# Performance work log

Hardware: AMD Instinct MI355X
Metric: run time of the kernel (lower is better)

## Reference

```python
import jax, jax.numpy as jnp
import numpy as np

N = 20000      # nodes
E = 160000     # edges
IN = 128       # in_channels
H = 16         # heads
C = 32         # hidden_channels (per-head dim)
HC = H * C     # 512
ED = 93        # edge_dim
B = 64         # graphs in batch


def setup_inputs() -> dict:
    key = jax.random.key(0)
    ks = jax.random.split(key, 32)
    w = lambda i, shape: jax.random.normal(ks[i], shape, dtype=jnp.float32) * 0.05
    inp = {
        "x": jax.random.normal(ks[0], (N, IN), dtype=jnp.float32),
        "edge_attr": jax.random.normal(ks[1], (E, ED), dtype=jnp.float32),
        "edge_index": jax.random.randint(ks[2], (2, E), 0, N),
        # sorted batch assignment; every graph id 0..B-1 is present
        "batch": (jnp.arange(N) * B) // N,
        # transformer1: in=IN
        "t1_Wq": w(3, (IN, HC)), "t1_bq": jnp.zeros((HC,), jnp.float32),
        "t1_Wk": w(4, (IN, HC)), "t1_bk": jnp.zeros((HC,), jnp.float32),
        "t1_Wv": w(5, (IN, HC)), "t1_bv": jnp.zeros((HC,), jnp.float32),
        "t1_We": w(6, (ED, HC)),
        "t1_Ws": w(7, (IN, HC)), "t1_bs": jnp.zeros((HC,), jnp.float32),
        # transformer2: in=HC
        "t2_Wq": w(8, (HC, HC)), "t2_bq": jnp.zeros((HC,), jnp.float32),
        "t2_Wk": w(9, (HC, HC)), "t2_bk": jnp.zeros((HC,), jnp.float32),
        "t2_Wv": w(10, (HC, HC)), "t2_bv": jnp.zeros((HC,), jnp.float32),
        "t2_We": w(11, (ED, HC)),
        "t2_Ws": w(12, (HC, HC)), "t2_bs": jnp.zeros((HC,), jnp.float32),
        # MLP head: fc1 (hidden*32 -> hidden*8), fc2 (hidden*8 -> hidden)
        "fc1_W": w(13, (2 * HC, 8 * C)), "fc1_b": jnp.zeros((8 * C,), jnp.float32),
        "fc2_W": w(14, (8 * C, C)), "fc2_b": jnp.zeros((C,), jnp.float32),
    }
    return inp


def _tconv(x, src, dst, edge_attr, Wq, bq, Wk, bk, Wv, bv, We, Ws, bs):
    # PyG TransformerConv, concat=True, beta=False, root_weight=True
    n = x.shape[0]
    q = (x @ Wq + bq).reshape(n, H, C)
    k = (x @ Wk + bk).reshape(n, H, C)
    v = (x @ Wv + bv).reshape(n, H, C)
    e = (edge_attr @ We).reshape(-1, H, C)          # lin_edge has no bias
    kj = k[src] + e                                  # [E,H,C]
    alpha = jnp.einsum('ehc,ehc->eh', q[dst], kj) / jnp.sqrt(jnp.float32(C))
    # segment softmax over incoming edges of each destination node
    amax = jax.ops.segment_max(alpha, dst, num_segments=n)
    ex = jnp.exp(alpha - amax[dst])
    denom = jax.ops.segment_sum(ex, dst, num_segments=n)
    a = ex / denom[dst]                              # [E,H]
    msg = (v[src] + e) * a[:, :, None]               # [E,H,C]
    agg = jax.ops.segment_sum(msg.reshape(-1, HC), dst, num_segments=n)
    return agg + x @ Ws + bs                         # root/skip connection


def _pool(x, batch):
    counts = jax.ops.segment_sum(jnp.ones((x.shape[0],), x.dtype), batch, num_segments=B)
    mean = jax.ops.segment_sum(x, batch, num_segments=B) / jnp.maximum(counts, 1.0)[:, None]
    mx = jax.ops.segment_max(x, batch, num_segments=B)
    return jnp.concatenate([mean, mx], axis=1)


def reference(x, edge_attr, edge_index, batch,
              t1_Wq, t1_bq, t1_Wk, t1_bk, t1_Wv, t1_bv, t1_We, t1_Ws, t1_bs,
              t2_Wq, t2_bq, t2_Wk, t2_bk, t2_Wv, t2_bv, t2_We, t2_Ws, t2_bs,
              fc1_W, fc1_b, fc2_W, fc2_b):
    src, dst = edge_index[0], edge_index[1]
    x1 = jax.nn.leaky_relu(_tconv(x, src, dst, edge_attr,
                                  t1_Wq, t1_bq, t1_Wk, t1_bk, t1_Wv, t1_bv,
                                  t1_We, t1_Ws, t1_bs), negative_slope=0.2)
    x3 = _pool(x1, batch)
    x2 = jax.nn.leaky_relu(_tconv(x1, src, dst, edge_attr,
                                  t2_Wq, t2_bq, t2_Wk, t2_bk, t2_Wv, t2_bv,
                                  t2_We, t2_Ws, t2_bs), negative_slope=0.2)
    x4 = _pool(x2, batch)
    h = x3 + x4                                      # [B, 2*HC]
    h = jax.nn.relu(h @ fc1_W + fc1_b)               # dropout = identity (eval)
    out = h @ fc2_W + fc2_b                          # [B, C]
    return out
```

## Files before the change

### kernel.cpp

```cpp
#include <hip/hip_runtime.h>
#include <cstdint>
#include <cstddef>

#define N_NODES 20000
#define N_EDGES 160000
#define IN_CH   128
#define NH      16
#define CD      32
#define HC      512
#define ED      93
#define EDP     96
#define NB      64
#define NCAT    2048
#define NSLICE  8
#define DEGSLK  2048

typedef __attribute__((ext_vector_type(8))) short short8;
typedef __attribute__((ext_vector_type(4))) float f32x4;
typedef unsigned short ushort_t;


__device__ inline ushort_t f2bf(float f) {
    unsigned int u = __float_as_uint(f);
    u = (u + 0x7FFF + ((u >> 16) & 1)) >> 16;
    return (ushort_t)u;
}
__device__ inline float bf2f(ushort_t u) {
    return __uint_as_float((unsigned)u << 16);
}
__device__ inline void unpack8(uint4 u, float* o) {
    o[0] = bf2f((ushort_t)(u.x & 0xffff)); o[1] = bf2f((ushort_t)(u.x >> 16));
    o[2] = bf2f((ushort_t)(u.y & 0xffff)); o[3] = bf2f((ushort_t)(u.y >> 16));
    o[4] = bf2f((ushort_t)(u.z & 0xffff)); o[5] = bf2f((ushort_t)(u.z >> 16));
    o[6] = bf2f((ushort_t)(u.w & 0xffff)); o[7] = bf2f((ushort_t)(u.w >> 16));
}
__device__ inline uint4 packf8(const float* f) {
    uint4 u;
    u.x = (unsigned)f2bf(f[0]) | ((unsigned)f2bf(f[1]) << 16);
    u.y = (unsigned)f2bf(f[2]) | ((unsigned)f2bf(f[3]) << 16);
    u.z = (unsigned)f2bf(f[4]) | ((unsigned)f2bf(f[5]) << 16);
    u.w = (unsigned)f2bf(f[6]) | ((unsigned)f2bf(f[7]) << 16);
    return u;
}

__device__ inline void gload_lds16(const void* g, void* l) {
    __builtin_amdgcn_global_load_lds(
        (const __attribute__((address_space(1))) void*)g,
        (__attribute__((address_space(3))) void*)l, 16, 0, 0);
}

__global__ void k_zero_i(int* __restrict__ p, int n) {
    int i = blockIdx.x * blockDim.x + threadIdx.x;
    int stride = gridDim.x * blockDim.x;
    for (; i < n; i += stride) p[i] = 0;
}

__global__ void k_cvt_x(const float* __restrict__ in, ushort_t* __restrict__ out, int n8) {
    int i = blockIdx.x * blockDim.x + threadIdx.x;
    int stride = gridDim.x * blockDim.x;
    for (; i < n8; i += stride) {
        const float4* p = (const float4*)(in + (size_t)i * 8);
        float4 a = p[0], b = p[1];
        float f[8] = {a.x, a.y, a.z, a.w, b.x, b.y, b.z, b.w};
        *(uint4*)(out + (size_t)i * 8) = packf8(f);
    }
}

__global__ void k_cvt_ea(const float* __restrict__ in, const int* __restrict__ perm,
                         ushort_t* __restrict__ out) {
    int i = blockIdx.x * blockDim.x + threadIdx.x;
    int stride = gridDim.x * blockDim.x;
    int total = N_EDGES * EDP;
    for (; i < total; i += stride) {
        int p = i / EDP, k = i - p * EDP;
        int e = perm[p];
        out[i] = (k < ED) ? f2bf(in[(size_t)e * ED + k]) : (ushort_t)0;
    }
}

__global__ __launch_bounds__(256) void k_cvt_wtT(
    const float* __restrict__ W0, const float* __restrict__ W1,
    const float* __restrict__ W2, const float* __restrict__ W3,
    ushort_t* __restrict__ Wt, int K, int N, int Kp) {
    __shared__ float tile[32][33];
    int z = blockIdx.z;
    const float* W = (z == 0) ? W0 : (z == 1) ? W1 : (z == 2) ? W2 : W3;
    ushort_t* out = Wt + (size_t)z * N * Kp;
    int n0 = blockIdx.x << 5;
    int k0 = blockIdx.y << 5;
    int r = threadIdx.x >> 5;
    int c = threadIdx.x & 31;
#pragma unroll
    for (int rr = 0; rr < 4; ++rr) {
        int k = k0 + r + rr * 8;
        tile[r + rr * 8][c] = (k < K) ? W[(size_t)k * N + n0 + c] : 0.f;
    }
    __syncthreads();
#pragma unroll
    for (int rr = 0; rr < 4; ++rr) {
        int n = n0 + r + rr * 8;
        out[(size_t)n * Kp + k0 + c] = f2bf(tile[c][r + rr * 8]);
    }
}

__global__ void k_bcat2(
    const float* __restrict__ b0q, const float* __restrict__ b0k,
    const float* __restrict__ b0v, const float* __restrict__ b0s,
    const float* __restrict__ b1q, const float* __restrict__ b1k,
    const float* __restrict__ b1v, const float* __restrict__ b1s,
    float* __restrict__ out) {
    int i = blockIdx.x * blockDim.x + threadIdx.x;
    if (i >= 2 * NCAT) return;
    int l = i >> 11, j = i & (NCAT - 1);
    int s = j >> 9, jj = j & 511;
    const float* b = (l == 0)
        ? ((s == 0) ? b0q : (s == 1) ? b0k : (s == 2) ? b0v : b0s)
        : ((s == 0) ? b1q : (s == 1) ? b1k : (s == 2) ? b1v : b1s);
    out[i] = b[jj];
}


__global__ void k_hist(const int* __restrict__ dst, int* __restrict__ deg) {
    int i = blockIdx.x * blockDim.x + threadIdx.x;
    if (i < N_EDGES) atomicAdd(&deg[dst[i]], 1);
}

__global__ __launch_bounds__(1024) void k_scan(const int* __restrict__ deg,
                                               int* __restrict__ rowptr,
                                               int* __restrict__ cursor) {
    __shared__ int part[1024];
    int t = threadIdx.x;
    int base = t * 20;
    int loc[20];
    int s = 0;
#pragma unroll
    for (int i = 0; i < 20; ++i) {
        int idx = base + i;
        int v = (idx < N_NODES) ? deg[idx] : 0;
        loc[i] = s; s += v;
    }
    part[t] = s;
    __syncthreads();
    for (int off = 1; off < 1024; off <<= 1) {
        int v = (t >= off) ? part[t - off] : 0;
        __syncthreads();
        part[t] += v;
        __syncthreads();
    }
    int pre = (t > 0) ? part[t - 1] : 0;
#pragma unroll
    for (int i = 0; i < 20; ++i) {
        int idx = base + i;
        if (idx < N_NODES) {
            int v = pre + loc[i];
            rowptr[idx] = v;
            cursor[idx] = v;
        }
    }
    if (t == 1023) rowptr[N_NODES] = part[1023];
}

__global__ void k_scatter(const int* __restrict__ src, const int* __restrict__ dst,
                          int* __restrict__ cursor, int* __restrict__ perm,
                          int* __restrict__ psrc) {
    int i = blockIdx.x * blockDim.x + threadIdx.x;
    if (i >= N_EDGES) return;
    int d = dst[i];
    int p = atomicAdd(&cursor[d], 1);
    perm[p] = i;
    psrc[p] = src[i];
}


__global__ __launch_bounds__(256) void k_mega(
    const ushort_t* __restrict__ A, const ushort_t* __restrict__ Bt,
    const float* __restrict__ bias, ushort_t* __restrict__ Yb,
    int M, int K, int N, int nq,
    const ushort_t* __restrict__ Ab, const ushort_t* __restrict__ Bte,
    ushort_t* __restrict__ Ybe, int ec, int neg) {
    __shared__ char smem[49152];
    int tid  = threadIdx.x;
    int lane = tid & 63, wave = tid >> 6;
    int l15 = lane & 15, lg = lane >> 4;
    int wm = (wave >> 1) * 64, wn = (wave & 1) * 64;

    if (blockIdx.x < nq) {
        char* As = smem;
        char* Bs = smem + 16384;
        int nt = N >> 7;
        int bid = blockIdx.x;
        int wg;
        if ((nq & 7) == 0) { int cpx = nq >> 3; wg = (bid & 7) * cpx + (bid >> 3); }
        else wg = bid;
        int bm = (wg / nt) * 128, bn = (wg % nt) * 128;

        f32x4 acc[4][4] = {};

        int sr = lane >> 3;
        int su = lane & 7;
        int gu = su ^ sr;

        for (int k0 = 0; k0 < K; k0 += 64) {
#pragma unroll
            for (int i = 0; i < 4; ++i) {
                int rloc = wave * 32 + i * 8;
                int row = rloc + sr;
                if (bm + row < M)
                    gload_lds16(A + (size_t)(bm + row) * K + k0 + gu * 8, As + rloc * 128);
                gload_lds16(Bt + (size_t)(bn + row) * K + k0 + gu * 8, Bs + rloc * 128);
            }
            __syncthreads();

#pragma unroll
            for (int ks = 0; ks < 2; ++ks) {
                short8 af[4], bfr[4];
#pragma unroll
                for (int mr = 0; mr < 4; ++mr) {
                    int r = wm + mr * 16 + l15;
                    af[mr] = *(const short8*)(As + r * 128 + (((ks * 4 + lg) ^ (r & 7)) << 4));
                }
#pragma unroll
                for (int nc = 0; nc < 4; ++nc) {
                    int r = wn + nc * 16 + l15;
                    bfr[nc] = *(const short8*)(Bs + r * 128 + (((ks * 4 + lg) ^ (r & 7)) << 4));
                }
#pragma unroll
                for (int mr = 0; mr < 4; ++mr)
#pragma unroll
                    for (int nc = 0; nc < 4; ++nc)
                        acc[mr][nc] = __builtin_amdgcn_mfma_f32_16x16x32_bf16(
                            af[mr], bfr[nc], acc[mr][nc], 0, 0, 0);
            }
            __syncthreads();
        }

        char* Cs = smem;
#pragma unroll
        for (int mr = 0; mr < 4; ++mr) {
#pragma unroll
            for (int nc = 0; nc < 4; ++nc) {
                int coll = wn + nc * 16 + l15;
                float b = bias ? bias[bn + coll] : 0.f;
                int u0 = coll >> 3;
#pragma unroll
                for (int j = 0; j < 4; ++j) {
                    int row = wm + mr * 16 + lg * 4 + j;
                    int u = u0 ^ (row & 7);
                    *(ushort_t*)(Cs + row * 256 + (u << 4) + ((coll & 7) << 1)) =
                        f2bf(acc[mr][nc][j] + b);
                }
            }
        }
        __syncthreads();
        {
            int rsub = tid >> 4;
            int un   = tid & 15;
#pragma unroll
            for (int i = 0; i < 8; ++i) {
                int row = i * 16 + rsub;
                int gr = bm + row;
                if (gr < M) {
                    int u = un ^ (row & 7);
                    *(uint4*)(Yb + (size_t)gr * N + bn + un * 8) =
                        *(const uint4*)(Cs + row * 256 + (u << 4));
                }
            }
        }
    } else {
        char* As = smem;
        char* Bs = smem + 24576;
        int bid = blockIdx.x - nq;
        int wg;
        if ((neg & 7) == 0) { int cpx = neg >> 3; wg = (bid & 7) * cpx + (bid >> 3); }
        else wg = bid;
        int bm = (wg >> 2) * 128;
        int n0 = (wg & 3) * 128;

        int srow = tid >> 1;
        int h    = tid & 1;
        int ssw  = ((srow >> 1) & 3) << 4;
        {
            int gm = bm + srow;
            uint4 va[6];
#pragma unroll
            for (int i = 0; i < 6; ++i) { va[i].x = va[i].y = va[i].z = va[i].w = 0; }
            if (gm < ec) {
                const uint4* ga = (const uint4*)(Ab + (size_t)gm * EDP + h * 48);
#pragma unroll
                for (int i = 0; i < 6; ++i) va[i] = ga[i];
            }
            char* dsta = As + srow * 192;
#pragma unroll
            for (int i = 0; i < 6; ++i) {
                int c = h * 96 + i * 16;
                *(uint4*)(dsta + ((c & ~63) | ((c & 63) ^ ssw))) = va[i];
            }
            uint4 vb[6];
            {
                const uint4* gb = (const uint4*)(Bte + (size_t)(n0 + srow) * EDP + h * 48);
#pragma unroll
                for (int i = 0; i < 6; ++i) vb[i] = gb[i];
            }
            char* dstb = Bs + srow * 192;
#pragma unroll
            for (int i = 0; i < 6; ++i) {
                int c = h * 96 + i * 16;
                *(uint4*)(dstb + ((c & ~63) | ((c & 63) ^ ssw))) = vb[i];
            }
        }
        __syncthreads();

        int fsw = ((l15 >> 1) & 3) << 4;

        f32x4 acc[4][4] = {};
#pragma unroll
        for (int ks = 0; ks < 3; ++ks) {
            short8 af[4], bfr[4];
#pragma unroll
            for (int mr = 0; mr < 4; ++mr) {
                int r = wm + mr * 16 + l15;
                int c = ks * 64 + ((lg * 16) ^ fsw);
                af[mr] = *(const short8*)(As + r * 192 + c);
            }
#pragma unroll
            for (int nc = 0; nc < 4; ++nc) {
                int r = wn + nc * 16 + l15;
                int c = ks * 64 + ((lg * 16) ^ fsw);
                bfr[nc] = *(const short8*)(Bs + r * 192 + c);
            }
#pragma unroll
            for (int mr = 0; mr < 4; ++mr)
#pragma unroll
                for (int nc = 0; nc < 4; ++nc)
                    acc[mr][nc] = __builtin_amdgcn_mfma_f32_16x16x32_bf16(
                        af[mr], bfr[nc], acc[mr][nc], 0, 0, 0);
        }
        __syncthreads();

        char* Cs = smem;
#pragma unroll
        for (int mr = 0; mr < 4; ++mr) {
#pragma unroll
            for (int nc = 0; nc < 4; ++nc) {
                int col = wn + nc * 16 + l15;
#pragma unroll
                for (int j = 0; j < 4; ++j) {
                    int row = wm + mr * 16 + lg * 4 + j;
                    *(ushort_t*)(Cs + row * 288 + col * 2) = f2bf(acc[mr][nc][j]);
                }
            }
        }
        __syncthreads();

        {
            int rsub = tid >> 4;
            int un   = tid & 15;
#pragma unroll
            for (int i = 0; i < 8; ++i) {
                int row = i * 16 + rsub;
                if (bm + row < ec) {
                    *(uint4*)(Ybe + (size_t)(bm + row) * HC + n0 + un * 8) =
                        *(const uint4*)(Cs + row * 288 + un * 16);
                }
            }
        }
    }
}


__global__ __launch_bounds__(256) void k_mfma_gemm(
    const ushort_t* __restrict__ A, const ushort_t* __restrict__ Bt,
    const float* __restrict__ bias, ushort_t* __restrict__ Yb,
    int M, int K, int N) {
    __shared__ char smem[32768];
    char* As = smem;
    char* Bs = smem + 16384;

    int tid  = threadIdx.x;
    int lane = tid & 63, wave = tid >> 6;
    int l15 = lane & 15, lg = lane >> 4;
    int nt = N >> 7;
    int nwg = gridDim.x;
    int bid = blockIdx.x;
    int wg;
    if ((nwg & 7) == 0) { int cpx = nwg >> 3; wg = (bid & 7) * cpx + (bid >> 3); }
    else wg = bid;
    int bm = (wg / nt) * 128, bn = (wg % nt) * 128;
    int wm = (wave >> 1) * 64, wn = (wave & 1) * 64;

    f32x4 acc[4][4] = {};

    int sr = lane >> 3;
    int su = lane & 7;
    int gu = su ^ sr;

    for (int k0 = 0; k0 < K; k0 += 64) {
#pragma unroll
        for (int i = 0; i < 4; ++i) {
            int rloc = wave * 32 + i * 8;
            int row = rloc + sr;
            if (bm + row < M)
                gload_lds16(A + (size_t)(bm + row) * K + k0 + gu * 8, As + rloc * 128);
            gload_lds16(Bt + (size_t)(bn + row) * K + k0 + gu * 8, Bs + rloc * 128);
        }
        __syncthreads();

#pragma unroll
        for (int ks = 0; ks < 2; ++ks) {
            short8 af[4], bfr[4];
#pragma unroll
            for (int mr = 0; mr < 4; ++mr) {
                int r = wm + mr * 16 + l15;
                af[mr] = *(const short8*)(As + r * 128 + (((ks * 4 + lg) ^ (r & 7)) << 4));
            }
#pragma unroll
            for (int nc = 0; nc < 4; ++nc) {
                int r = wn + nc * 16 + l15;
                bfr[nc] = *(const short8*)(Bs + r * 128 + (((ks * 4 + lg) ^ (r & 7)) << 4));
            }
#pragma unroll
            for (int mr = 0; mr < 4; ++mr)
#pragma unroll
                for (int nc = 0; nc < 4; ++nc)
                    acc[mr][nc] = __builtin_amdgcn_mfma_f32_16x16x32_bf16(
                        af[mr], bfr[nc], acc[mr][nc], 0, 0, 0);
        }
        __syncthreads();
    }

    char* Cs = smem;
#pragma unroll
    for (int mr = 0; mr < 4; ++mr) {
#pragma unroll
        for (int nc = 0; nc < 4; ++nc) {
            int coll = wn + nc * 16 + l15;
            float b = bias ? bias[bn + coll] : 0.f;
            int u0 = coll >> 3;
#pragma unroll
            for (int j = 0; j < 4; ++j) {
                int row = wm + mr * 16 + lg * 4 + j;
                int u = u0 ^ (row & 7);
                *(ushort_t*)(Cs + row * 256 + (u << 4) + ((coll & 7) << 1)) =
                    f2bf(acc[mr][nc][j] + b);
            }
        }
    }
    __syncthreads();
    {
        int rsub = tid >> 4;
        int un   = tid & 15;
#pragma unroll
        for (int i = 0; i < 8; ++i) {
            int row = i * 16 + rsub;
            int gr = bm + row;
            if (gr < M) {
                int u = un ^ (row & 7);
                *(uint4*)(Yb + (size_t)gr * N + bn + un * 8) =
                    *(const uint4*)(Cs + row * 256 + (u << 4));
            }
        }
    }
}


__global__ __launch_bounds__(256) void k_egemm(
    const ushort_t* __restrict__ Ab, const ushort_t* __restrict__ Bt,
    ushort_t* __restrict__ Yb, int pbase, int ec) {
    __shared__ char smem[49152];
    char* As = smem;
    char* Bs = smem + 24576;

    int tid  = threadIdx.x;
    int lane = tid & 63, wave = tid >> 6;
    int l15 = lane & 15, lg = lane >> 4;
    int nwg = gridDim.x;
    int bid = blockIdx.x;
    int wg;
    if ((nwg & 7) == 0) { int cpx = nwg >> 3; wg = (bid & 7) * cpx + (bid >> 3); }
    else wg = bid;
    int bm = (wg >> 2) * 128;
    int n0 = (wg & 3) * 128;
    int wm = (wave >> 1) * 64, wn = (wave & 1) * 64;

    int srow = tid >> 1;
    int h    = tid & 1;
    int ssw  = ((srow >> 1) & 3) << 4;
    {
        int gm = bm + srow;
        uint4 va[6];
#pragma unroll
        for (int i = 0; i < 6; ++i) { va[i].x = va[i].y = va[i].z = va[i].w = 0; }
        if (gm < ec) {
            const uint4* ga = (const uint4*)(Ab + (size_t)(pbase + gm) * EDP + h * 48);
#pragma unroll
            for (int i = 0; i < 6; ++i) va[i] = ga[i];
        }
        char* dsta = As + srow * 192;
#pragma unroll
        for (int i = 0; i < 6; ++i) {
            int c = h * 96 + i * 16;
            *(uint4*)(dsta + ((c & ~63) | ((c & 63) ^ ssw))) = va[i];
        }
        uint4 vb[6];
        {
            const uint4* gb = (const uint4*)(Bt + (size_t)(n0 + srow) * EDP + h * 48);
#pragma unroll
            for (int i = 0; i < 6; ++i) vb[i] = gb[i];
        }
        char* dstb = Bs + srow * 192;
#pragma unroll
        for (int i = 0; i < 6; ++i) {
            int c = h * 96 + i * 16;
            *(uint4*)(dstb + ((c & ~63) | ((c & 63) ^ ssw))) = vb[i];
        }
    }
    __syncthreads();

    int fsw = ((l15 >> 1) & 3) << 4;

    f32x4 acc[4][4] = {};
#pragma unroll
    for (int ks = 0; ks < 3; ++ks) {
        short8 af[4], bfr[4];
#pragma unroll
        for (int mr = 0; mr < 4; ++mr) {
            int r = wm + mr * 16 + l15;
            int c = ks * 64 + ((lg * 16) ^ fsw);
            af[mr] = *(const short8*)(As + r * 192 + c);
        }
#pragma unroll
        for (int nc = 0; nc < 4; ++nc) {
            int r = wn + nc * 16 + l15;
            int c = ks * 64 + ((lg * 16) ^ fsw);
            bfr[nc] = *(const short8*)(Bs + r * 192 + c);
        }
#pragma unroll
        for (int mr = 0; mr < 4; ++mr)
#pragma unroll
            for (int nc = 0; nc < 4; ++nc)
                acc[mr][nc] = __builtin_amdgcn_mfma_f32_16x16x32_bf16(
                    af[mr], bfr[nc], acc[mr][nc], 0, 0, 0);
    }
    __syncthreads();

    char* Cs = smem;
#pragma unroll
    for (int mr = 0; mr < 4; ++mr) {
#pragma unroll
        for (int nc = 0; nc < 4; ++nc) {
            int col = wn + nc * 16 + l15;
#pragma unroll
            for (int j = 0; j < 4; ++j) {
                int row = wm + mr * 16 + lg * 4 + j;
                *(ushort_t*)(Cs + row * 288 + col * 2) = f2bf(acc[mr][nc][j]);
            }
        }
    }
    __syncthreads();

    {
        int rsub = tid >> 4;
        int un   = tid & 15;
#pragma unroll
        for (int i = 0; i < 8; ++i) {
            int row = i * 16 + rsub;
            if (bm + row < ec) {
                *(uint4*)(Yb + (size_t)(bm + row) * HC + n0 + un * 8) =
                    *(const uint4*)(Cs + row * 288 + un * 16);
            }
        }
    }
}


__global__ __launch_bounds__(128) void k_edge_fc(
    const ushort_t* __restrict__ qkvs, const ushort_t* __restrict__ eb,
    const int* __restrict__ psrc, const int* __restrict__ rowptr,
    ushort_t* __restrict__ xoutb, int e0, int elim) {
    int n = blockIdx.x;
    int beg = rowptr[n], end = rowptr[n + 1];
    if (beg < e0 || beg >= elim) return;

    int t = threadIdx.x;
    int w = t >> 6;
    int lane = t & 63;
    int c0 = lane * 8;
    int h = lane >> 2;

    float q[8];
    unpack8(*(const uint4*)(qkvs + (size_t)n * NCAT + c0), q);

    float mm = -1e30f, dd = 0.f, a[8];
#pragma unroll
    for (int j = 0; j < 8; ++j) a[j] = 0.f;

    int i = beg + w;
    uint4 ku4, vu4, eu4;
    if (i < end) {
        int sn = psrc[i];
        ku4 = *(const uint4*)(qkvs + (size_t)sn * NCAT + 512 + c0);
        vu4 = *(const uint4*)(qkvs + (size_t)sn * NCAT + 1024 + c0);
        eu4 = *(const uint4*)(eb + (size_t)(i - e0) * HC + c0);
    }
    while (i < end) {
        uint4 kc = ku4, vc = vu4, ec = eu4;
        int inext = i + 2;
        if (inext < end) {
            int sn2 = psrc[inext];
            ku4 = *(const uint4*)(qkvs + (size_t)sn2 * NCAT + 512 + c0);
            vu4 = *(const uint4*)(qkvs + (size_t)sn2 * NCAT + 1024 + c0);
            eu4 = *(const uint4*)(eb + (size_t)(inext - e0) * HC + c0);
        }
        float kk[8], vv[8], ee[8];
        unpack8(kc, kk); unpack8(vc, vv); unpack8(ec, ee);
        float part = 0.f;
#pragma unroll
        for (int j = 0; j < 8; ++j) part += q[j] * (kk[j] + ee[j]);
        part += __shfl_xor(part, 1);
        part += __shfl_xor(part, 2);
        float s = part * 0.17677669529663687f;
        float mn = fmaxf(mm, s);
        float sc = __expf(mm - mn);
        float p  = __expf(s - mn);
        dd = dd * sc + p;
        mm = mn;
#pragma unroll
        for (int j = 0; j < 8; ++j) a[j] = a[j] * sc + p * (vv[j] + ee[j]);
        i = inext;
    }

    __shared__ float sm_acc[512];
    __shared__ float sm_m[16];
    __shared__ float sm_d[16];
    if (w == 1) {
#pragma unroll
        for (int j = 0; j < 8; ++j) sm_acc[c0 + j] = a[j];
        if ((lane & 3) == 0) { sm_m[h] = mm; sm_d[h] = dd; }
    }
    __syncthreads();
    if (w == 0) {
        float m1 = sm_m[h], d1 = sm_d[h];
        float M = fmaxf(mm, m1);
        float sc0 = __expf(mm - M);
        float sc1 = __expf(m1 - M);
        dd = dd * sc0 + d1 * sc1;
        float inv = (dd > 0.f) ? 1.f / dd : 0.f;
        float sk[8];
        unpack8(*(const uint4*)(qkvs + (size_t)n * NCAT + 1536 + c0), sk);
        float o[8];
#pragma unroll
        for (int j = 0; j < 8; ++j) {
            float msg = (a[j] * sc0 + sm_acc[c0 + j] * sc1) * inv;
            float v = msg + sk[j];
            o[j] = v >= 0.f ? v : 0.2f * v;
        }
        *(uint4*)(xoutb + (size_t)n * HC + c0) = packf8(o);
    }
}


__global__ __launch_bounds__(256) void k_pool2(
    const ushort_t* __restrict__ xb, const int* __restrict__ batch,
    float* __restrict__ psum_p, float* __restrict__ pmax_p, int* __restrict__ cnt) {
    int b = blockIdx.x;
    int s = blockIdx.y;
    int lo = 0, hi = N_NODES;
    while (lo < hi) { int mid = (lo + hi) >> 1; if (batch[mid] < b) lo = mid + 1; else hi = mid; }
    int beg = lo;
    hi = N_NODES;
    while (lo < hi) { int mid = (lo + hi) >> 1; if (batch[mid] < b + 1) lo = mid + 1; else hi = mid; }
    int end = lo;
    if (s == 0 && threadIdx.x == 0) cnt[b] = end - beg;
    int cn = end - beg;
    int per = (cn + NSLICE - 1) / NSLICE;
    int nb = beg + s * per;
    int ne = nb + per; if (ne > end) ne = end;
    int c0 = threadIdx.x * 2;
    float s0 = 0.f, s1 = 0.f, m0 = -1e30f, m1 = -1e30f;
    for (int n = nb; n < ne; ++n) {
        unsigned int v = *(const unsigned int*)(xb + (size_t)n * HC + c0);
        float v0 = bf2f((ushort_t)(v & 0xffff));
        float v1 = bf2f((ushort_t)(v >> 16));
        s0 += v0; s1 += v1;
        m0 = fmaxf(m0, v0); m1 = fmaxf(m1, v1);
    }
    size_t o = ((size_t)s * NB + b) * HC + c0;
    psum_p[o] = s0; psum_p[o + 1] = s1;
    pmax_p[o] = m0; pmax_p[o + 1] = m1;
}

__global__ void k_poolfin(const float* __restrict__ psum_p, const float* __restrict__ pmax_p,
                          const int* __restrict__ cnt, float* __restrict__ hsum, int mode) {
    int i = blockIdx.x * blockDim.x + threadIdx.x;
    if (i >= NB * 1024) return;
    int b = i >> 10, c = i & 1023;
    float val;
    if (c < HC) {
        float s = 0.f;
#pragma unroll
        for (int sl = 0; sl < NSLICE; ++sl)
            s += psum_p[((size_t)sl * NB + b) * HC + c];
        int ct = cnt[b];
        val = s / (float)(ct > 0 ? ct : 1);
    } else {
        int cc = c - HC;
        float m = -1e30f;
#pragma unroll
        for (int sl = 0; sl < NSLICE; ++sl)
            m = fmaxf(m, pmax_p[((size_t)sl * NB + b) * HC + cc]);
        val = m;
    }
    if (mode == 0) hsum[i] = val;
    else hsum[i] += val;
}


__global__ __launch_bounds__(256) void k_head(
    const float* __restrict__ hsum, const float* __restrict__ fc1W,
    const float* __restrict__ fc1b, const float* __restrict__ fc2W,
    const float* __restrict__ fc2b, float* __restrict__ out) {
    int b = blockIdx.x;
    int j = threadIdx.x;
    __shared__ float hs[256];
    float acc = fc1b[j];
    const float* hin = hsum + (size_t)b * 1024;
    for (int k = 0; k < 1024; ++k) {
        acc += hin[k] * fc1W[(size_t)k * 256 + j];
    }
    hs[j] = fmaxf(acc, 0.f);
    __syncthreads();
    if (j < 32) {
        float o = fc2b[j];
        for (int k = 0; k < 256; ++k) o += hs[k] * fc2W[(size_t)k * 32 + j];
        out[b * 32 + j] = o;
    }
}


extern "C" void kernel_launch(void* const* d_in, const int* in_sizes, int n_in,
                              void* d_out, int out_size, void* d_ws, size_t ws_size,
                              hipStream_t stream) {
    const float* x      = (const float*)d_in[0];
    const float* ea     = (const float*)d_in[1];
    const int*   ei     = (const int*)d_in[2];
    const int*   batch  = (const int*)d_in[3];
    const int* src = ei;
    const int* dst = ei + N_EDGES;

    const float* t1_Wq = (const float*)d_in[4];
    const float* t1_bq = (const float*)d_in[5];
    const float* t1_Wk = (const float*)d_in[6];
    const float* t1_bk = (const float*)d_in[7];
    const float* t1_Wv = (const float*)d_in[8];
    const float* t1_bv = (const float*)d_in[9];
    const float* t1_We = (const float*)d_in[10];
    const float* t1_Ws = (const float*)d_in[11];
    const float* t1_bs = (const float*)d_in[12];
    const float* t2_Wq = (const float*)d_in[13];
    const float* t2_bq = (const float*)d_in[14];
    const float* t2_Wk = (const float*)d_in[15];
    const float* t2_bk = (const float*)d_in[16];
    const float* t2_Wv = (const float*)d_in[17];
    const float* t2_bv = (const float*)d_in[18];
    const float* t2_We = (const float*)d_in[19];
    const float* t2_Ws = (const float*)d_in[20];
    const float* t2_bs = (const float*)d_in[21];
    const float* fc1_W = (const float*)d_in[22];
    const float* fc1_b = (const float*)d_in[23];
    const float* fc2_W = (const float*)d_in[24];
    const float* fc2_b = (const float*)d_in[25];

    char* ws = (char*)d_ws;
    size_t off = 0;
    auto alloc = [&](size_t bytes) -> void* {
        void* p = ws + off;
        off = (off + bytes + 255) & ~(size_t)255;
        return p;
    };

    ushort_t* qkvs = (ushort_t*)alloc((size_t)N_NODES * NCAT * 2);
    float* psum_p = (float*)alloc((size_t)NSLICE * NB * HC * 4);
    float* pmax_p = (float*)alloc((size_t)NSLICE * NB * HC * 4);
    float* hsum = (float*)alloc((size_t)NB * 1024 * 4);
    int*   cnt  = (int*)alloc((size_t)NB * 4);
    int* deg    = (int*)alloc((size_t)N_NODES * 4);
    int* rowptr = (int*)alloc((size_t)(N_NODES + 1) * 4);
    int* cursor = (int*)alloc((size_t)N_NODES * 4);
    int* perm   = (int*)alloc((size_t)N_EDGES * 4);
    int* psrc   = (int*)alloc((size_t)N_EDGES * 4);
    ushort_t* x_b  = (ushort_t*)alloc((size_t)N_NODES * IN_CH * 2);
    ushort_t* x1_b = (ushort_t*)alloc((size_t)N_NODES * HC * 2);
    ushort_t* ea_b = (ushort_t*)alloc((size_t)N_EDGES * EDP * 2);
    ushort_t* wcat1 = (ushort_t*)alloc((size_t)NCAT * IN_CH * 2);
    ushort_t* wcat2 = (ushort_t*)alloc((size_t)NCAT * HC * 2);
    ushort_t* w_e   = (ushort_t*)alloc((size_t)2 * HC * EDP * 2);
    float* bcat = (float*)alloc((size_t)2 * NCAT * 4);

    size_t remain = (ws_size > off) ? (ws_size - off) : 0;
    ushort_t* eb = (ushort_t*)(ws + off);
    size_t per_edge = (size_t)HC * 2;
    long cap_rows = (long)(remain / per_edge);
    long S_max = cap_rows - DEGSLK;
    if (S_max < 1024) S_max = 1024;
    int nch = (int)((N_EDGES + S_max - 1) / S_max);
    if (nch < 1) nch = 1;
    int S = (N_EDGES + nch - 1) / nch;
    (void)in_sizes; (void)n_in; (void)out_size;

    hipLaunchKernelGGL(k_zero_i, dim3(79), dim3(256), 0, stream, deg, N_NODES);
    hipLaunchKernelGGL(k_hist, dim3((N_EDGES + 255) / 256), dim3(256), 0, stream, dst, deg);
    hipLaunchKernelGGL(k_scan, dim3(1), dim3(1024), 0, stream, deg, rowptr, cursor);
    hipLaunchKernelGGL(k_scatter, dim3((N_EDGES + 255) / 256), dim3(256), 0, stream,
                       src, dst, cursor, perm, psrc);

    hipLaunchKernelGGL(k_cvt_x, dim3(512), dim3(256), 0, stream, x, x_b,
                       N_NODES * IN_CH / 8);
    hipLaunchKernelGGL(k_cvt_ea, dim3(4096), dim3(256), 0, stream, ea, perm, ea_b);
    hipLaunchKernelGGL(k_cvt_wtT, dim3(HC / 32, IN_CH / 32, 4), dim3(256), 0, stream,
                       t1_Wq, t1_Wk, t1_Wv, t1_Ws, wcat1, IN_CH, HC, IN_CH);
    hipLaunchKernelGGL(k_cvt_wtT, dim3(HC / 32, HC / 32, 4), dim3(256), 0, stream,
                       t2_Wq, t2_Wk, t2_Wv, t2_Ws, wcat2, HC, HC, HC);
    hipLaunchKernelGGL(k_cvt_wtT, dim3(HC / 32, EDP / 32, 2), dim3(256), 0, stream,
                       t1_We, t2_We, t1_We, t1_We, w_e, ED, HC, EDP);
    hipLaunchKernelGGL(k_bcat2, dim3(16), dim3(256), 0, stream,
                       t1_bq, t1_bk, t1_bv, t1_bs, t2_bq, t2_bk, t2_bv, t2_bs, bcat);

    auto run_layer = [&](const ushort_t* xin_b, int Kin, const ushort_t* wcat,
                         const float* bc, const ushort_t* we,
                         ushort_t* xoutb, int poolmode) {
        int mt = (N_NODES + 127) / 128;
        int nt = NCAT / 128;
        int nq = mt * nt;

        long ecl0 = (long)S + DEGSLK;
        if (ecl0 > N_EDGES) ecl0 = N_EDGES;
        int ecnt0 = (int)ecl0;
        int neg0 = ((ecnt0 + 127) / 128) * 4;
        hipLaunchKernelGGL(k_mega, dim3(nq + neg0), dim3(256), 0, stream,
                           xin_b, wcat, bc, qkvs, N_NODES, Kin, NCAT, nq,
                           ea_b, we, eb, ecnt0, neg0);
        {
            int elim0 = (nch == 1) ? (N_EDGES + 1) : S;
            hipLaunchKernelGGL(k_edge_fc, dim3(N_NODES), dim3(128), 0, stream,
                               qkvs, eb, psrc, rowptr, xoutb, 0, elim0);
        }
        for (int ci = 1; ci < nch; ++ci) {
            int e0 = ci * S;
            if (e0 >= N_EDGES) break;
            long ecl = (long)S + DEGSLK;
            if (ecl > N_EDGES - e0) ecl = N_EDGES - e0;
            int ecnt = (int)ecl;
            int gm = (ecnt + 127) / 128;
            hipLaunchKernelGGL(k_egemm, dim3(gm * 4), dim3(256), 0, stream,
                               ea_b, we, eb, e0, ecnt);
            int elim = (ci == nch - 1) ? (N_EDGES + 1) : (e0 + S);
            hipLaunchKernelGGL(k_edge_fc, dim3(N_NODES), dim3(128), 0, stream,
                               qkvs, eb, psrc, rowptr, xoutb, e0, elim);
        }

        hipLaunchKernelGGL(k_pool2, dim3(NB, NSLICE), dim3(256), 0, stream,
                           xoutb, batch, psum_p, pmax_p, cnt);
        hipLaunchKernelGGL(k_poolfin, dim3((NB * 1024 + 255) / 256), dim3(256), 0, stream,
                           psum_p, pmax_p, cnt, hsum, poolmode);
    };

    run_layer(x_b, IN_CH, wcat1, bcat, w_e, x1_b, 0);
    run_layer(x1_b, HC, wcat2, bcat + NCAT, w_e + (size_t)HC * EDP, x1_b, 1);

    hipLaunchKernelGGL(k_head, dim3(NB), dim3(256), 0, stream,
                       hsum, fc1_W, fc1_b, fc2_W, fc2_b, (float*)d_out);
}
```

Measured before the change: 545.6 us.

## Fuse edge attention with next-chunk edge GEMM using double-buffered edge features

Replaces the separate edge-GEMM and edge-attention kernels with one kernel whose grid holds attention blocks for the current chunk (two nodes per 256-thread block) plus GEMM blocks that produce the next chunk's edge features into a second buffer. The aim is to overlap the edge projection with the gather-heavy attention and cut kernel launches. Chunk count is now picked so that two chunk buffers fit in the workspace. If the workspace holds all edges, nothing changes except the two-node-per-block packing, and smaller chunks may mean more launches when the workspace is tight.

```diff
diff --git a/kernel.cpp b/kernel.cpp
--- a/kernel.cpp
+++ b/kernel.cpp
@@ -14,6 +14,7 @@
 #define NCAT    2048
 #define NSLICE  8
 #define DEGSLK  2048
+#define NPAIR   10000
 
 typedef __attribute__((ext_vector_type(8))) short short8;
 typedef __attribute__((ext_vector_type(4))) float f32x4;
@@ -184,7 +185,7 @@
     int l15 = lane & 15, lg = lane >> 4;
     int wm = (wave >> 1) * 64, wn = (wave & 1) * 64;
 
-    if (blockIdx.x < nq) {
+    if ((int)blockIdx.x < nq) {
         char* As = smem;
         char* Bs = smem + 16384;
         int nt = N >> 7;
@@ -368,55 +369,160 @@
 }
 
 
-__global__ __launch_bounds__(256) void k_mfma_gemm(
-    const ushort_t* __restrict__ A, const ushort_t* __restrict__ Bt,
-    const float* __restrict__ bias, ushort_t* __restrict__ Yb,
-    int M, int K, int N) {
-    __shared__ char smem[32768];
-    char* As = smem;
-    char* Bs = smem + 16384;
-
+__global__ __launch_bounds__(256) void k_pipe(
+    const ushort_t* __restrict__ qkvs, const ushort_t* __restrict__ ebR,
+    const int* __restrict__ psrc, const int* __restrict__ rowptr,
+    ushort_t* __restrict__ xoutb, int e0, int elim, int npair,
+    const ushort_t* __restrict__ Ab, const ushort_t* __restrict__ Bte,
+    ushort_t* __restrict__ ebW, int pbase2, int ec2, int neg2) {
+    __shared__ char smem[49152];
     int tid  = threadIdx.x;
-    int lane = tid & 63, wave = tid >> 6;
-    int l15 = lane & 15, lg = lane >> 4;
-    int nt = N >> 7;
-    int nwg = gridDim.x;
-    int bid = blockIdx.x;
-    int wg;
-    if ((nwg & 7) == 0) { int cpx = nwg >> 3; wg = (bid & 7) * cpx + (bid >> 3); }
-    else wg = bid;
-    int bm = (wg / nt) * 128, bn = (wg % nt) * 128;
-    int wm = (wave >> 1) * 64, wn = (wave & 1) * 64;
-
-    f32x4 acc[4][4] = {};
-
-    int sr = lane >> 3;
-    int su = lane & 7;
-    int gu = su ^ sr;
-
-    for (int k0 = 0; k0 < K; k0 += 64) {
-#pragma unroll
-        for (int i = 0; i < 4; ++i) {
-            int rloc = wave * 32 + i * 8;
-            int row = rloc + sr;
-            if (bm + row < M)
-                gload_lds16(A + (size_t)(bm + row) * K + k0 + gu * 8, As + rloc * 128);
-            gload_lds16(Bt + (size_t)(bn + row) * K + k0 + gu * 8, Bs + rloc * 128);
-        }
-        __syncthreads();
-
-#pragma unroll
-        for (int ks = 0; ks < 2; ++ks) {
+
+    if ((int)blockIdx.x < npair) {
+        int half = tid >> 7;
+        int t    = tid & 127;
+        int w    = t >> 6;
+        int lane = t & 63;
+        int c0 = lane * 8;
+        int h = lane >> 2;
+        int n = blockIdx.x * 2 + half;
+        int beg = rowptr[n], end = rowptr[n + 1];
+        bool act = (beg >= e0 && beg < elim);
+
+        float q[8];
+        unpack8(*(const uint4*)(qkvs + (size_t)n * NCAT + c0), q);
+
+        float mm = -1e30f, dd = 0.f, a[8];
+#pragma unroll
+        for (int j = 0; j < 8; ++j) a[j] = 0.f;
+
+        int iend = act ? end : 0;
+        int i = (act ? beg : 0) + w;
+        uint4 ku4, vu4, eu4;
+        if (i < iend) {
+            int sn = psrc[i];
+            ku4 = *(const uint4*)(qkvs + (size_t)sn * NCAT + 512 + c0);
+            vu4 = *(const uint4*)(qkvs + (size_t)sn * NCAT + 1024 + c0);
+            eu4 = *(const uint4*)(ebR + (size_t)(i - e0) * HC + c0);
+        }
+        while (i < iend) {
+            uint4 kc = ku4, vc = vu4, ec = eu4;
+            int inext = i + 2;
+            if (inext < iend) {
+                int sn2 = psrc[inext];
+                ku4 = *(const uint4*)(qkvs + (size_t)sn2 * NCAT + 512 + c0);
+                vu4 = *(const uint4*)(qkvs + (size_t)sn2 * NCAT + 1024 + c0);
+                eu4 = *(const uint4*)(ebR + (size_t)(inext - e0) * HC + c0);
+            }
+            float kk[8], vv[8], ee[8];
+            unpack8(kc, kk); unpack8(vc, vv); unpack8(ec, ee);
+            float part = 0.f;
+#pragma unroll
+            for (int j = 0; j < 8; ++j) part += q[j] * (kk[j] + ee[j]);
+            part += __shfl_xor(part, 1);
+            part += __shfl_xor(part, 2);
+            float s = part * 0.17677669529663687f;
+            float mn = fmaxf(mm, s);
+            float sc = __expf(mm - mn);
+            float p  = __expf(s - mn);
+            dd = dd * sc + p;
+            mm = mn;
+#pragma unroll
+            for (int j = 0; j < 8; ++j) a[j] = a[j] * sc + p * (vv[j] + ee[j]);
+            i = inext;
+        }
+
+        float* sm_acc = (float*)smem + (size_t)half * 512;
+        float* sm_m   = (float*)(smem + 4096) + half * 16;
+        float* sm_d   = (float*)(smem + 4096 + 128) + half * 16;
+        if (w == 1) {
+#pragma unroll
+            for (int j = 0; j < 8; ++j) sm_acc[c0 + j] = a[j];
+            if ((lane & 3) == 0) { sm_m[h] = mm; sm_d[h] = dd; }
+        }
+        __syncthreads();
+        if (w == 0 && act) {
+            float m1 = sm_m[h], d1 = sm_d[h];
+            float M = fmaxf(mm, m1);
+            float sc0 = __expf(mm - M);
+            float sc1 = __expf(m1 - M);
+            dd = dd * sc0 + d1 * sc1;
+            float inv = (dd > 0.f) ? 1.f / dd : 0.f;
+            float sk[8];
+            unpack8(*(const uint4*)(qkvs + (size_t)n * NCAT + 1536 + c0), sk);
+            float o[8];
+#pragma unroll
+            for (int j = 0; j < 8; ++j) {
+                float msg = (a[j] * sc0 + sm_acc[c0 + j] * sc1) * inv;
+                float v = msg + sk[j];
+                o[j] = v >= 0.f ? v : 0.2f * v;
+            }
+            *(uint4*)(xoutb + (size_t)n * HC + c0) = packf8(o);
+        }
+    } else {
+        int lane = tid & 63, wave = tid >> 6;
+        int l15 = lane & 15, lg = lane >> 4;
+        int wm = (wave >> 1) * 64, wn = (wave & 1) * 64;
+        char* As = smem;
+        char* Bs = smem + 24576;
+        int bid = blockIdx.x - npair;
+        int wg;
+        if ((neg2 & 7) == 0) { int cpx = neg2 >> 3; wg = (bid & 7) * cpx + (bid >> 3); }
+        else wg = bid;
+        int bm = (wg >> 2) * 128;
+        int n0 = (wg & 3) * 128;
+
+        int srow = tid >> 1;
+        int h    = tid & 1;
+        int ssw  = ((srow >> 1) & 3) << 4;
+        {
+            int gm = bm + srow;
+            uint4 va[6];
+#pragma unroll
+            for (int i = 0; i < 6; ++i) { va[i].x = va[i].y = va[i].z = va[i].w = 0; }
+            if (gm < ec2) {
+                const uint4* ga = (const uint4*)(Ab + (size_t)(pbase2 + gm) * EDP + h * 48);
+#pragma unroll
+                for (int i = 0; i < 6; ++i) va[i] = ga[i];
+            }
+            char* dsta = As + srow * 192;
+#pragma unroll
+            for (int i = 0; i < 6; ++i) {
+                int c = h * 96 + i * 16;
+                *(uint4*)(dsta + ((c & ~63) | ((c & 63) ^ ssw))) = va[i];
+            }
+            uint4 vb[6];
+            {
+                const uint4* gb = (const uint4*)(Bte + (size_t)(n0 + srow) * EDP + h * 48);
+#pragma unroll
+                for (int i = 0; i < 6; ++i) vb[i] = gb[i];
+            }
+            char* dstb = Bs + srow * 192;
+#pragma unroll
+            for (int i = 0; i < 6; ++i) {
+                int c = h * 96 + i * 16;
+                *(uint4*)(dstb + ((c & ~63) | ((c & 63) ^ ssw))) = vb[i];
+            }
+        }
+        __syncthreads();
+
+        int fsw = ((l15 >> 1) & 3) << 4;
+
+        f32x4 acc[4][4] = {};
+#pragma unroll
+        for (int ks = 0; ks < 3; ++ks) {
             short8 af[4], bfr[4];
 #pragma unroll
             for (int mr = 0; mr < 4; ++mr) {
                 int r = wm + mr * 16 + l15;
-                af[mr] = *(const short8*)(As + r * 128 + (((ks * 4 + lg) ^ (r & 7)) << 4));
+                int c = ks * 64 + ((lg * 16) ^ fsw);
+                af[mr] = *(const short8*)(As + r * 192 + c);
             }
 #pragma unroll
             for (int nc = 0; nc < 4; ++nc) {
                 int r = wn + nc * 16 + l15;
-                bfr[nc] = *(const short8*)(Bs + r * 128 + (((ks * 4 + lg) ^ (r & 7)) << 4));
+                int c = ks * 64 + ((lg * 16) ^ fsw);
+                bfr[nc] = *(const short8*)(Bs + r * 192 + c);
             }
 #pragma unroll
             for (int mr = 0; mr < 4; ++mr)
@@ -426,235 +532,34 @@
                         af[mr], bfr[nc], acc[mr][nc], 0, 0, 0);
         }
         __syncthreads();
-    }
-
-    char* Cs = smem;
-#pragma unroll
-    for (int mr = 0; mr < 4; ++mr) {
-#pragma unroll
-        for (int nc = 0; nc < 4; ++nc) {
-            int coll = wn + nc * 16 + l15;
-            float b = bias ? bias[bn + coll] : 0.f;
-            int u0 = coll >> 3;
-#pragma unroll
-            for (int j = 0; j < 4; ++j) {
-                int row = wm + mr * 16 + lg * 4 + j;
-                int u = u0 ^ (row & 7);
-                *(ushort_t*)(Cs + row * 256 + (u << 4) + ((coll & 7) << 1)) =
-                    f2bf(acc[mr][nc][j] + b);
-            }
-        }
-    }
-    __syncthreads();
-    {
-        int rsub = tid >> 4;
-        int un   = tid & 15;
-#pragma unroll
-        for (int i = 0; i < 8; ++i) {
-            int row = i * 16 + rsub;
-            int gr = bm + row;
-            if (gr < M) {
-                int u = un ^ (row & 7);
-                *(uint4*)(Yb + (size_t)gr * N + bn + un * 8) =
-                    *(const uint4*)(Cs + row * 256 + (u << 4));
-            }
-        }
-    }
-}
-
-
-__global__ __launch_bounds__(256) void k_egemm(
-    const ushort_t* __restrict__ Ab, const ushort_t* __restrict__ Bt,
-    ushort_t* __restrict__ Yb, int pbase, int ec) {
-    __shared__ char smem[49152];
-    char* As = smem;
-    char* Bs = smem + 24576;
-
-    int tid  = threadIdx.x;
-    int lane = tid & 63, wave = tid >> 6;
-    int l15 = lane & 15, lg = lane >> 4;
-    int nwg = gridDim.x;
-    int bid = blockIdx.x;
-    int wg;
-    if ((nwg & 7) == 0) { int cpx = nwg >> 3; wg = (bid & 7) * cpx + (bid >> 3); }
-    else wg = bid;
-    int bm = (wg >> 2) * 128;
-    int n0 = (wg & 3) * 128;
-    int wm = (wave >> 1) * 64, wn = (wave & 1) * 64;
-
-    int srow = tid >> 1;
-    int h    = tid & 1;
-    int ssw  = ((srow >> 1) & 3) << 4;
-    {
-        int gm = bm + srow;
-        uint4 va[6];
-#pragma unroll
-        for (int i = 0; i < 6; ++i) { va[i].x = va[i].y = va[i].z = va[i].w = 0; }
-        if (gm < ec) {
-            const uint4* ga = (const uint4*)(Ab + (size_t)(pbase + gm) * EDP + h * 48);
-#pragma unroll
-            for (int i = 0; i < 6; ++i) va[i] = ga[i];
-        }
-        char* dsta = As + srow * 192;
-#pragma unroll
-        for (int i = 0; i < 6; ++i) {
-            int c = h * 96 + i * 16;
-            *(uint4*)(dsta + ((c & ~63) | ((c & 63) ^ ssw))) = va[i];
-        }
-        uint4 vb[6];
+
+        char* Cs = smem;
+#pragma unroll
+        for (int mr = 0; mr < 4; ++mr) {
+#pragma unroll
+            for (int nc = 0; nc < 4; ++nc) {
+                int col = wn + nc * 16 + l15;
+#pragma unroll
+                for (int j = 0; j < 4; ++j) {
+                    int row = wm + mr * 16 + lg * 4 + j;
+                    *(ushort_t*)(Cs + row * 288 + col * 2) = f2bf(acc[mr][nc][j]);
+                }
+            }
+        }
+        __syncthreads();
+
         {
-            const uint4* gb = (const uint4*)(Bt + (size_t)(n0 + srow) * EDP + h * 48);
-#pragma unroll
-            for (int i = 0; i < 6; ++i) vb[i] = gb[i];
-        }
-        char* dstb = Bs + srow * 192;
-#pragma unroll
-        for (int i = 0; i < 6; ++i) {
-            int c = h * 96 + i * 16;
-            *(uint4*)(dstb + ((c & ~63) | ((c & 63) ^ ssw))) = vb[i];
-        }
-    }
-    __syncthreads();
-
-    int fsw = ((l15 >> 1) & 3) << 4;
-
-    f32x4 acc[4][4] = {};
-#pragma unroll
-    for (int ks = 0; ks < 3; ++ks) {
-        short8 af[4], bfr[4];
-#pragma unroll
-        for (int mr = 0; mr < 4; ++mr) {
-            int r = wm + mr * 16 + l15;
-            int c = ks * 64 + ((lg * 16) ^ fsw);
-            af[mr] = *(const short8*)(As + r * 192 + c);
-        }
-#pragma unroll
-        for (int nc = 0; nc < 4; ++nc) {
-            int r = wn + nc * 16 + l15;
-            int c = ks * 64 + ((lg * 16) ^ fsw);
-            bfr[nc] = *(const short8*)(Bs + r * 192 + c);
-        }
-#pragma unroll
-        for (int mr = 0; mr < 4; ++mr)
-#pragma unroll
-            for (int nc = 0; nc < 4; ++nc)
-                acc[mr][nc] = __builtin_amdgcn_mfma_f32_16x16x32_bf16(
-                    af[mr], bfr[nc], acc[mr][nc], 0, 0, 0);
-    }
-    __syncthreads();
-
-    char* Cs = smem;
-#pragma unroll
-    for (int mr = 0; mr < 4; ++mr) {
-#pragma unroll
-        for (int nc = 0; nc < 4; ++nc) {
-            int col = wn + nc * 16 + l15;
-#pragma unroll
-            for (int j = 0; j < 4; ++j) {
-                int row = wm + mr * 16 + lg * 4 + j;
-                *(ushort_t*)(Cs + row * 288 + col * 2) = f2bf(acc[mr][nc][j]);
-            }
-        }
-    }
-    __syncthreads();
-
-    {
-        int rsub = tid >> 4;
-        int un   = tid & 15;
-#pragma unroll
-        for (int i = 0; i < 8; ++i) {
-            int row = i * 16 + rsub;
-            if (bm + row < ec) {
-                *(uint4*)(Yb + (size_t)(bm + row) * HC + n0 + un * 8) =
-                    *(const uint4*)(Cs + row * 288 + un * 16);
-            }
-        }
-    }
-}
-
-
-__global__ __launch_bounds__(128) void k_edge_fc(
-    const ushort_t* __restrict__ qkvs, const ushort_t* __restrict__ eb,
-    const int* __restrict__ psrc, const int* __restrict__ rowptr,
-    ushort_t* __restrict__ xoutb, int e0, int elim) {
-    int n = blockIdx.x;
-    int beg = rowptr[n], end = rowptr[n + 1];
-    if (beg < e0 || beg >= elim) return;
-
-    int t = threadIdx.x;
-    int w = t >> 6;
-    int lane = t & 63;
-    int c0 = lane * 8;
-    int h = lane >> 2;
-
-    float q[8];
-    unpack8(*(const uint4*)(qkvs + (size_t)n * NCAT + c0), q);
-
-    float mm = -1e30f, dd = 0.f, a[8];
-#pragma unroll
-    for (int j = 0; j < 8; ++j) a[j] = 0.f;
-
-    int i = beg + w;
-    uint4 ku4, vu4, eu4;
-    if (i < end) {
-        int sn = psrc[i];
-        ku4 = *(const uint4*)(qkvs + (size_t)sn * NCAT + 512 + c0);
-        vu4 = *(const uint4*)(qkvs + (size_t)sn * NCAT + 1024 + c0);
-        eu4 = *(const uint4*)(eb + (size_t)(i - e0) * HC + c0);
-    }
-    while (i < end) {
-        uint4 kc = ku4, vc = vu4, ec = eu4;
-        int inext = i + 2;
-        if (inext < end) {
-            int sn2 = psrc[inext];
-            ku4 = *(const uint4*)(qkvs + (size_t)sn2 * NCAT + 512 + c0);
-            vu4 = *(const uint4*)(qkvs + (size_t)sn2 * NCAT + 1024 + c0);
-            eu4 = *(const uint4*)(eb + (size_t)(inext - e0) * HC + c0);
-        }
-        float kk[8], vv[8], ee[8];
-        unpack8(kc, kk); unpack8(vc, vv); unpack8(ec, ee);
-        float part = 0.f;
-#pragma unroll
-        for (int j = 0; j < 8; ++j) part += q[j] * (kk[j] + ee[j]);
-        part += __shfl_xor(part, 1);
-        part += __shfl_xor(part, 2);
-        float s = part * 0.17677669529663687f;
-        float mn = fmaxf(mm, s);
-        float sc = __expf(mm - mn);
-        float p  = __expf(s - mn);
-        dd = dd * sc + p;
-        mm = mn;
-#pragma unroll
-        for (int j = 0; j < 8; ++j) a[j] = a[j] * sc + p * (vv[j] + ee[j]);
-        i = inext;
-    }
-
-    __shared__ float sm_acc[512];
-    __shared__ float sm_m[16];
-    __shared__ float sm_d[16];
-    if (w == 1) {
-#pragma unroll
-        for (int j = 0; j < 8; ++j) sm_acc[c0 + j] = a[j];
-        if ((lane & 3) == 0) { sm_m[h] = mm; sm_d[h] = dd; }
-    }
-    __syncthreads();
-    if (w == 0) {
-        float m1 = sm_m[h], d1 = sm_d[h];
-        float M = fmaxf(mm, m1);
-        float sc0 = __expf(mm - M);
-        float sc1 = __expf(m1 - M);
-        dd = dd * sc0 + d1 * sc1;
-        float inv = (dd > 0.f) ? 1.f / dd : 0.f;
-        float sk[8];
-        unpack8(*(const uint4*)(qkvs + (size_t)n * NCAT + 1536 + c0), sk);
-        float o[8];
-#pragma unroll
-        for (int j = 0; j < 8; ++j) {
-            float msg = (a[j] * sc0 + sm_acc[c0 + j] * sc1) * inv;
-            float v = msg + sk[j];
-            o[j] = v >= 0.f ? v : 0.2f * v;
-        }
-        *(uint4*)(xoutb + (size_t)n * HC + c0) = packf8(o);
+            int rsub = tid >> 4;
+            int un   = tid & 15;
+#pragma unroll
+            for (int i = 0; i < 8; ++i) {
+                int row = i * 16 + rsub;
+                if (bm + row < ec2) {
+                    *(uint4*)(ebW + (size_t)(bm + row) * HC + n0 + un * 8) =
+                        *(const uint4*)(Cs + row * 288 + un * 16);
+                }
+            }
+        }
     }
 }
 
@@ -797,14 +702,21 @@
     float* bcat = (float*)alloc((size_t)2 * NCAT * 4);
 
     size_t remain = (ws_size > off) ? (ws_size - off) : 0;
-    ushort_t* eb = (ushort_t*)(ws + off);
     size_t per_edge = (size_t)HC * 2;
     long cap_rows = (long)(remain / per_edge);
-    long S_max = cap_rows - DEGSLK;
-    if (S_max < 1024) S_max = 1024;
-    int nch = (int)((N_EDGES + S_max - 1) / S_max);
-    if (nch < 1) nch = 1;
+    int nch = -1;
+    if (cap_rows >= (long)N_EDGES) nch = 1;
+    else {
+        for (int c = 2; c <= 64; ++c) {
+            long s = (N_EDGES + c - 1) / c;
+            if (2 * (s + DEGSLK) <= cap_rows) { nch = c; break; }
+        }
+        if (nch < 0) nch = 64;
+    }
     int S = (N_EDGES + nch - 1) / nch;
+    size_t bufrows = (nch == 1) ? (size_t)N_EDGES : (size_t)(S + DEGSLK);
+    ushort_t* ebA = (ushort_t*)(ws + off);
+    ushort_t* ebB = (nch == 1) ? ebA : ebA + bufrows * HC;
     (void)in_sizes; (void)n_in; (void)out_size;
 
     hipLaunchKernelGGL(k_zero_i, dim3(79), dim3(256), 0, stream, deg, N_NODES);
@@ -832,30 +744,32 @@
         int nt = NCAT / 128;
         int nq = mt * nt;
 
-        long ecl0 = (long)S + DEGSLK;
-        if (ecl0 > N_EDGES) ecl0 = N_EDGES;
-        int ecnt0 = (int)ecl0;
-        int neg0 = ((ecnt0 + 127) / 128) * 4;
+        int ec0 = (nch == 1) ? N_EDGES
+                             : (int)((S + DEGSLK < N_EDGES) ? (S + DEGSLK) : N_EDGES);
+        int neg0 = ((ec0 + 127) / 128) * 4;
         hipLaunchKernelGGL(k_mega, dim3(nq + neg0), dim3(256), 0, stream,
                            xin_b, wcat, bc, qkvs, N_NODES, Kin, NCAT, nq,
-                           ea_b, we, eb, ecnt0, neg0);
-        {
-            int elim0 = (nch == 1) ? (N_EDGES + 1) : S;
-            hipLaunchKernelGGL(k_edge_fc, dim3(N_NODES), dim3(128), 0, stream,
-                               qkvs, eb, psrc, rowptr, xoutb, 0, elim0);
-        }
-        for (int ci = 1; ci < nch; ++ci) {
+                           ea_b, we, ebA, ec0, neg0);
+
+        for (int ci = 0; ci < nch; ++ci) {
             int e0 = ci * S;
             if (e0 >= N_EDGES) break;
-            long ecl = (long)S + DEGSLK;
-            if (ecl > N_EDGES - e0) ecl = N_EDGES - e0;
-            int ecnt = (int)ecl;
-            int gm = (ecnt + 127) / 128;
-            hipLaunchKernelGGL(k_egemm, dim3(gm * 4), dim3(256), 0, stream,
-                               ea_b, we, eb, e0, ecnt);
+            ushort_t* ebR = ((ci & 1) == 0) ? ebA : ebB;
             int elim = (ci == nch - 1) ? (N_EDGES + 1) : (e0 + S);
-            hipLaunchKernelGGL(k_edge_fc, dim3(N_NODES), dim3(128), 0, stream,
-                               qkvs, eb, psrc, rowptr, xoutb, e0, elim);
+            int cj = ci + 1;
+            int neg2 = 0, pb2 = 0, ec2 = 0;
+            ushort_t* ebW = ebA;
+            if (cj < nch && cj * S < N_EDGES) {
+                pb2 = cj * S;
+                long ecl = (long)S + DEGSLK;
+                if (ecl > N_EDGES - pb2) ecl = N_EDGES - pb2;
+                ec2 = (int)ecl;
+                neg2 = ((ec2 + 127) / 128) * 4;
+                ebW = ((cj & 1) == 0) ? ebA : ebB;
+            }
+            hipLaunchKernelGGL(k_pipe, dim3(NPAIR + neg2), dim3(256), 0, stream,
+                               qkvs, ebR, psrc, rowptr, xoutb, e0, elim, NPAIR,
+                               ea_b, we, ebW, pb2, ec2, neg2);
         }
 
         hipLaunchKernelGGL(k_pool2, dim3(NB, NSLICE), dim3(256), 0, stream,
```

Result: slower. 587.1 us (+7.6%).
